# Performance work log

Measured on AMD Instinct MI355X. Metric: run time of the kernel, lower is better.

## Reference

```python
import jax, jax.numpy as jnp
import numpy as np

N = 50000          # nodes
E = 1250000        # edges (no self loops in raw data)
H = 2              # heads
C = 32             # out channels per head
DIN = 64           # dim_node
ED = 16            # edge_dim
G = 16             # graphs in batch
NC = 5             # num classes
SLOPE = 0.2        # GATConv leaky_relu negative_slope


def _glorot(key, shape):
    fan = shape[0] if len(shape) == 2 else shape[-1]
    return jax.random.normal(key, shape, jnp.float32) * (1.0 / np.sqrt(fan))


def setup_inputs() -> dict:
    key = jax.random.key(0)
    ks = jax.random.split(key, 24)
    x = jax.random.normal(ks[0], (N, DIN), jnp.float32)
    dst = jax.random.randint(ks[1], (E,), 0, N)
    off = jax.random.randint(ks[2], (E,), 1, N)
    src = (dst + off) % N  # guarantees src != dst (PyG removes self loops before re-adding)
    edge_index = jnp.stack([src, dst]).astype(jnp.int32)
    edge_attr = jax.random.normal(ks[3], (E, ED), jnp.float32)
    batch = jnp.sort(jax.random.randint(ks[4], (N,), 0, G)).astype(jnp.int32)
    inp = dict(x=x, edge_index=edge_index, edge_attr=edge_attr, batch=batch)
    # layer 1: in=DIN, heads=H, out=C, concat -> H*C
    inp["W1"] = _glorot(ks[5], (DIN, H * C)); inp["asrc1"] = _glorot(ks[6], (H, C))
    inp["adst1"] = _glorot(ks[7], (H, C)); inp["We1"] = _glorot(ks[8], (ED, H * C))
    inp["ae1"] = _glorot(ks[9], (H, C)); inp["b1"] = jnp.zeros((H * C,), jnp.float32)
    # layer 2: in=H*C, heads=H, out=C, concat
    inp["W2"] = _glorot(ks[10], (H * C, H * C)); inp["asrc2"] = _glorot(ks[11], (H, C))
    inp["adst2"] = _glorot(ks[12], (H, C)); inp["We2"] = _glorot(ks[13], (ED, H * C))
    inp["ae2"] = _glorot(ks[14], (H, C)); inp["b2"] = jnp.zeros((H * C,), jnp.float32)
    # layer 3: in=H*C, heads=1, out=C, concat=False
    inp["W3"] = _glorot(ks[15], (H * C, C)); inp["asrc3"] = _glorot(ks[16], (1, C))
    inp["adst3"] = _glorot(ks[17], (1, C)); inp["We3"] = _glorot(ks[18], (ED, C))
    inp["ae3"] = _glorot(ks[19], (1, C)); inp["b3"] = jnp.zeros((C,), jnp.float32)
    # ffn: Linear(C, NC) + softmax (dropout is identity in eval)
    inp["Wf"] = _glorot(ks[20], (C, NC)); inp["bf"] = jnp.zeros((NC,), jnp.float32)
    return inp


def _gat_layer(h_in, src, dst, eattr, W, asrc, adst, We, ae, b, heads, out, concat):
    n = h_in.shape[0]
    h = (h_in @ W).reshape(n, heads, out)                      # [N,H,C]
    s_src = jnp.einsum('nhc,hc->nh', h, asrc)                  # per-node src scores
    s_dst = jnp.einsum('nhc,hc->nh', h, adst)
    he = (eattr @ We).reshape(-1, heads, out)                  # [E,H,C]
    s_e = jnp.einsum('ehc,hc->eh', he, ae)
    logit = jax.nn.leaky_relu(s_src[src] + s_dst[dst] + s_e, SLOPE)  # [E,H]
    m = jax.ops.segment_max(logit, dst, num_segments=n)
    ex = jnp.exp(logit - m[dst])
    den = jax.ops.segment_sum(ex, dst, num_segments=n)
    alpha = ex / (den[dst] + 1e-16)                            # segment softmax per dst node
    agg = jax.ops.segment_sum(h[src] * alpha[..., None], dst, num_segments=n)  # [N,H,C]
    out_x = agg.reshape(n, heads * out) if concat else agg.mean(axis=1)
    return out_x + b


def _gat_forward(x, edge_index, edge_attr, batch,
                 W1, asrc1, adst1, We1, ae1, b1,
                 W2, asrc2, adst2, We2, ae2, b2,
                 W3, asrc3, adst3, We3, ae3, b3,
                 Wf, bf):
    src, dst = edge_index[0], edge_index[1]
    n = x.shape[0]
    # add_self_loops with fill_value='mean': self-loop edge_attr = mean of incoming edge_attr
    deg = jax.ops.segment_sum(jnp.ones((src.shape[0],), x.dtype), dst, num_segments=n)
    self_attr = jax.ops.segment_sum(edge_attr, dst, num_segments=n) / jnp.maximum(deg, 1.0)[:, None]
    loop = jnp.arange(n, dtype=src.dtype)
    src_a = jnp.concatenate([src, loop])
    dst_a = jnp.concatenate([dst, loop])
    eattr_a = jnp.concatenate([edge_attr, self_attr], axis=0)

    h = jax.nn.relu(_gat_layer(x, src_a, dst_a, eattr_a, W1, asrc1, adst1, We1, ae1, b1, H, C, True))
    h = jax.nn.relu(_gat_layer(h, src_a, dst_a, eattr_a, W2, asrc2, adst2, We2, ae2, b2, H, C, True))
    h = jax.nn.relu(_gat_layer(h, src_a, dst_a, eattr_a, W3, asrc3, adst3, We3, ae3, b3, 1, C, False))

    # global mean pool per graph
    cnt = jax.ops.segment_sum(jnp.ones((n,), h.dtype), batch, num_segments=G)
    pooled = jax.ops.segment_sum(h, batch, num_segments=G) / jnp.maximum(cnt, 1.0)[:, None]
    # ffn: Dropout (identity at eval) -> Linear -> Softmax(dim=1)
    return jax.nn.softmax(pooled @ Wf + bf, axis=1)


def reference(x, edge_index, edge_attr, batch,
              W1, asrc1, adst1, We1, ae1, b1,
              W2, asrc2, adst2, We2, ae2, b2,
              W3, asrc3, adst3, We3, ae3, b3,
              Wf, bf):
    return _gat_forward(x, edge_index, edge_attr, batch,
                        W1, asrc1, adst1, We1, ae1, b1,
                        W2, asrc2, adst2, We2, ae2, b2,
                        W3, asrc3, adst3, We3, ae3, b3,
                        Wf, bf)
```

## Files before the change

kernel.cpp:

```cpp
#include <hip/hip_runtime.h>
#include <math.h>

#define NN 50000
#define EE 1250000
#define GG 16
#define NCLS 5
#define NBIN 391
#define BINSHIFT 7
#define CAPB 3900
#define NABLK 153
#define NTBLK 3125

constexpr size_t AL(size_t x){ return (x + 255) & ~size_t(255); }
constexpr size_t OFF_ROWPTR = 0;
constexpr size_t OFF_SRCS   = OFF_ROWPTR + AL((size_t)(NN+1)*4);
constexpr size_t OFF_SE12   = OFF_SRCS + AL((size_t)EE*2);
constexpr size_t OFF_SE34   = OFF_SE12 + AL((size_t)EE*4);
constexpr size_t OFF_SE5    = OFF_SE34 + AL((size_t)EE*4);
constexpr size_t OFF_SSRCA  = OFF_SE5 + AL((size_t)EE*2);
constexpr size_t OFF_SDSTA  = OFF_SSRCA + AL((size_t)NN*2*4);
constexpr size_t OFF_SSRCB  = OFF_SDSTA + AL((size_t)NN*2*4);
constexpr size_t OFF_SDSTB  = OFF_SSRCB + AL((size_t)NN*2*4);
constexpr size_t OFF_STAG   = OFF_SDSTB + AL((size_t)NN*2*4);
constexpr size_t OFF_BUFHA  = OFF_STAG + AL((size_t)NBIN*CAPB*16);
constexpr size_t OFF_BUFHB  = OFF_BUFHA + AL((size_t)NN*32*4);
constexpr size_t OFF_BUFO   = OFF_BUFHB + AL((size_t)NN*32*4);
constexpr size_t OFF_POOL   = OFF_BUFO + AL((size_t)NN*32*4);

__device__ __forceinline__ float leaky(float x){ return x > 0.f ? x : 0.2f*x; }
__device__ __forceinline__ unsigned rne_bf16(float x){
    unsigned u = __float_as_uint(x);
    return (u + 0x7FFFu + ((u >> 16) & 1u)) >> 16;
}
__device__ __forceinline__ float bf16lo(unsigned p){ return __uint_as_float(p << 16); }
__device__ __forceinline__ float bf16hi(unsigned p){ return __uint_as_float(p & 0xFFFF0000u); }

__global__ __launch_bounds__(1024)
void binAt1_kernel(const int* __restrict__ src, const int* __restrict__ dst,
                   const float* __restrict__ eattr,
                   const float* __restrict__ We1, const float* __restrict__ ae1,
                   const float* __restrict__ We2, const float* __restrict__ ae2,
                   const float* __restrict__ We3, const float* __restrict__ ae3,
                   int* __restrict__ bincursor, int4* __restrict__ staging,
                   const float* __restrict__ x, const float* __restrict__ W1,
                   const float* __restrict__ asrc1, const float* __restrict__ adst1,
                   unsigned* __restrict__ hout2, float* __restrict__ ssrc,
                   float* __restrict__ sdst, int nE, int nN){
    __shared__ float smem[5120];
    int tid = threadIdx.x;

    if (blockIdx.x >= NABLK){
        float* Ws  = smem;
        float* ins = smem + 4096;
        for (int i = tid; i < 4096; i += 1024) Ws[i] = W1[i];
        int base = (blockIdx.x - NABLK) * 16;
        {
            int n = base + (tid >> 6);
            ins[tid] = (n < nN) ? x[(size_t)n*64 + (tid & 63)] : 0.f;
        }
        __syncthreads();
        int r = tid >> 6, c = tid & 63;
        int n = base + r;
        float acc = 0.f;
        #pragma unroll
        for (int d = 0; d < 64; ++d) acc += ins[r*64 + d] * Ws[d*64 + c];
        float ps = acc * asrc1[c];
        float pd = acc * adst1[c];
        #pragma unroll
        for (int m = 1; m <= 16; m <<= 1){ ps += __shfl_xor(ps, m); pd += __shfl_xor(pd, m); }
        float accN = __shfl_xor(acc, 1);
        if (n < nN){
            if ((c & 1) == 0){
                unsigned pk = rne_bf16(acc) | (rne_bf16(accN) << 16);
                hout2[(size_t)n*32 + (c >> 1)] = pk;
            }
            if ((c & 31) == 0){
                int h = c >> 5;
                ssrc[n*2 + h] = ps;
                sdst[n*2 + h] = pd;
            }
        }
        return;
    }

    int*   lcount = (int*)smem;
    int*   lbase  = lcount + NBIN;
    float* w      = (float*)(lbase + NBIN);
    if (tid < 80){
        int j = tid >> 4, d = tid & 15;
        const float* We; const float* ae; int hc, h;
        if (j == 0){ We = We1; ae = ae1; hc = 64; h = 0; }
        else if (j == 1){ We = We1; ae = ae1; hc = 64; h = 1; }
        else if (j == 2){ We = We2; ae = ae2; hc = 64; h = 0; }
        else if (j == 3){ We = We2; ae = ae2; hc = 64; h = 1; }
        else { We = We3; ae = ae3; hc = 32; h = 0; }
        float s = 0.f;
        for (int c = 0; c < 32; ++c) s += We[d*hc + h*32 + c] * ae[h*32 + c];
        w[tid] = s;
    }
    for (int i = tid; i < NBIN; i += 1024) lcount[i] = 0;
    __syncthreads();
    int base = blockIdx.x * 8192;
    int w0[8], bn[8], idx[8]; unsigned p01[8], p23[8], p4[8];
    #pragma unroll
    for (int k = 0; k < 8; ++k){
        int i = base + k*1024 + tid;
        if (i < nE){
            int d = dst[i];
            int s = src[i];
            bn[k]  = d >> BINSHIFT;
            w0[k]  = s | ((d & 127) << 16);
            const float4* row = (const float4*)(eattr + (size_t)i*16);
            float4 a0 = row[0], a1 = row[1], a2 = row[2], a3 = row[3];
            float a[16] = {a0.x,a0.y,a0.z,a0.w, a1.x,a1.y,a1.z,a1.w,
                           a2.x,a2.y,a2.z,a2.w, a3.x,a3.y,a3.z,a3.w};
            float sj[5];
            #pragma unroll
            for (int j = 0; j < 5; ++j){
                float s2 = 0.f;
                #pragma unroll
                for (int d2 = 0; d2 < 16; ++d2) s2 += a[d2]*w[j*16+d2];
                sj[j] = s2;
            }
            p01[k] = rne_bf16(sj[0]) | (rne_bf16(sj[1]) << 16);
            p23[k] = rne_bf16(sj[2]) | (rne_bf16(sj[3]) << 16);
            p4[k]  = rne_bf16(sj[4]);
            idx[k] = atomicAdd(&lcount[bn[k]], 1);
        } else bn[k] = -1;
    }
    __syncthreads();
    for (int i = tid; i < NBIN; i += 1024){
        int c = lcount[i];
        lbase[i] = c ? (i*CAPB + atomicAdd(&bincursor[i], c)) : 0;
    }
    __syncthreads();
    #pragma unroll
    for (int k = 0; k < 8; ++k)
        if (bn[k] >= 0)
            staging[lbase[bn[k]] + idx[k]] = make_int4(w0[k], (int)p01[k], (int)p23[k], (int)p4[k]);
}

__global__ void binB_kernel(const int* __restrict__ bincursor, const int4* __restrict__ staging,
                            unsigned short* __restrict__ srcs, unsigned* __restrict__ se12,
                            unsigned* __restrict__ se34, unsigned short* __restrict__ se5,
                            int* __restrict__ rowptr, int nN){
    __shared__ int4 lout[CAPB];
    __shared__ int lcnt[128];
    __shared__ int lpre[128];
    __shared__ int sbb;
    int b = blockIdx.x;
    int sbase = b*CAPB;
    int cnt = bincursor[b];
    int tid = threadIdx.x;
    if (tid < 128) lcnt[tid] = 0;
    if (tid < 64){
        int sum = 0;
        for (int i = tid; i < b; i += 64) sum += bincursor[i];
        #pragma unroll
        for (int m = 1; m < 64; m <<= 1) sum += __shfl_xor(sum, m);
        if (tid == 0) sbb = sum;
    }
    __syncthreads();
    for (int k = tid; k < cnt; k += 1024)
        atomicAdd(&lcnt[staging[sbase + k].x >> 16], 1);
    __syncthreads();
    if (tid < 64){
        int a0 = lcnt[2*tid], a1 = lcnt[2*tid+1];
        int pair = a0 + a1, incl = pair;
        #pragma unroll
        for (int off = 1; off < 64; off <<= 1){
            int t = __shfl_up(incl, off);
            if (tid >= off) incl += t;
        }
        int base0 = incl - pair;
        lpre[2*tid] = base0;
        lpre[2*tid+1] = base0 + a0;
    }
    __syncthreads();
    int r0 = sbb;
    int lo = b << BINSHIFT;
    if (tid < 128 && lo + tid < nN) rowptr[lo + tid] = r0 + lpre[tid];
    if (b == 0 && tid == 0) rowptr[nN] = EE;
    if (tid < 128) lcnt[tid] = 0;
    __syncthreads();
    for (int k = tid; k < cnt; k += 1024){
        int4 v = staging[sbase + k];
        int dl = v.x >> 16;
        int rank = atomicAdd(&lcnt[dl], 1);
        v.x &= 0xFFFF;
        lout[lpre[dl] + rank] = v;
    }
    __syncthreads();
    for (int k = tid; k < cnt; k += 1024){
        int4 v = lout[k];
        srcs[r0 + k] = (unsigned short)v.x;
        se12[r0 + k] = (unsigned)v.y;
        se34[r0 + k] = (unsigned)v.z;
        se5[r0 + k]  = (unsigned short)v.w;
    }
}

template<int NEXTC>
__global__ __launch_bounds__(1024)
void agg64f_kernel(const int* __restrict__ rowptr, const unsigned short* __restrict__ srcs,
                   const unsigned* __restrict__ sePa,
                   const float* __restrict__ ssrc, const float* __restrict__ sdst,
                   const unsigned* __restrict__ hbuf2, const float* __restrict__ bias,
                   const float* __restrict__ Wn, const float* __restrict__ asrcn,
                   const float* __restrict__ adstn,
                   unsigned* __restrict__ houtn, float* __restrict__ ssrcn,
                   float* __restrict__ sdstn, int nN){
    __shared__ float WnS[64*NEXTC];
    __shared__ float os[16*64];
    int tid = threadIdx.x;
    int wid = tid >> 6;
    int lane = tid & 63;
    for (int i = tid; i < 64*NEXTC; i += 1024) WnS[i] = Wn[i];
    int n = blockIdx.x*16 + wid;

    int row_start = rowptr[n], row_end = rowptr[n+1];
    int degn = row_end - row_start;
    float sd0 = sdst[n*2 + 0];
    float sd1 = sdst[n*2 + 1];
    int sub = lane >> 4;
    int lc  = lane & 15;
    int h   = lc >> 3;
    float acc0=0.f, acc1=0.f, acc2=0.f, acc3=0.f, den=0.f;
    float ssp0=0.f, ssp1=0.f;
    const uint2* hb2 = (const uint2*)hbuf2;

    for (int p0 = row_start; p0 < row_end; p0 += 64){
        int myp = p0 + lane;
        int srcreg = 0; unsigned wpk = 0;
        if (myp < row_end){
            srcreg = srcs[myp];
            unsigned pk = sePa[myp];
            float e0 = bf16lo(pk);
            float e1 = bf16hi(pk);
            ssp0 += e0; ssp1 += e1;
            float2 sv = ((const float2*)ssrc)[srcreg];
            float w0 = __expf(leaky(sv.x + sd0 + e0));
            float w1 = __expf(leaky(sv.y + sd1 + e1));
            wpk = rne_bf16(w0) | (rne_bf16(w1) << 16);
        }
        int cnt = min(64, row_end - p0);
        #pragma unroll 4
        for (int q = sub; q < cnt; q += 4){
            int sj = __shfl(srcreg, q);
            unsigned wq = __shfl(wpk, q);
            float wj = h ? bf16hi(wq) : bf16lo(wq);
            den += wj;
            uint2 hv = hb2[(size_t)sj*16 + lc];
            acc0 += wj * bf16lo(hv.x);
            acc1 += wj * bf16hi(hv.x);
            acc2 += wj * bf16lo(hv.y);
            acc3 += wj * bf16hi(hv.y);
        }
    }
    #pragma unroll
    for (int m = 16; m < 64; m <<= 1){
        acc0 += __shfl_xor(acc0, m); acc1 += __shfl_xor(acc1, m);
        acc2 += __shfl_xor(acc2, m); acc3 += __shfl_xor(acc3, m);
        den  += __shfl_xor(den, m);
    }
    #pragma unroll
    for (int m = 1; m < 64; m <<= 1){
        ssp0 += __shfl_xor(ssp0, m);
        ssp1 += __shfl_xor(ssp1, m);
    }
    float invdeg = 1.f / (float)max(degn, 1);
    float srh = ssrc[n*2 + h];
    float sdh = h ? sd1 : sd0;
    float ssh = h ? ssp1 : ssp0;
    float wself = __expf(leaky(srh + sdh + ssh*invdeg));
    uint2 hv = hb2[(size_t)n*16 + lc];
    acc0 += wself * bf16lo(hv.x); acc1 += wself * bf16hi(hv.x);
    acc2 += wself * bf16lo(hv.y); acc3 += wself * bf16hi(hv.y);
    den += wself;
    if (lane < 16){
        float inv = 1.f / (den + 1e-16f);
        os[wid*64 + 4*lc+0] = fmaxf(acc0*inv + bias[4*lc+0], 0.f);
        os[wid*64 + 4*lc+1] = fmaxf(acc1*inv + bias[4*lc+1], 0.f);
        os[wid*64 + 4*lc+2] = fmaxf(acc2*inv + bias[4*lc+2], 0.f);
        os[wid*64 + 4*lc+3] = fmaxf(acc3*inv + bias[4*lc+3], 0.f);
    }
    __syncthreads();
    if (NEXTC == 64){
        int c = lane;
        float hh = 0.f;
        #pragma unroll
        for (int d = 0; d < 64; ++d) hh += os[wid*64 + d] * WnS[d*64 + c];
        float ps = hh * asrcn[c];
        float pd = hh * adstn[c];
        #pragma unroll
        for (int m = 1; m <= 16; m <<= 1){ ps += __shfl_xor(ps, m); pd += __shfl_xor(pd, m); }
        float hN = __shfl_xor(hh, 1);
        if ((c & 1) == 0){
            unsigned pk = rne_bf16(hh) | (rne_bf16(hN) << 16);
            houtn[(size_t)n*32 + (c >> 1)] = pk;
        }
        if ((c & 31) == 0){
            int hh2 = c >> 5;
            ssrcn[n*2 + hh2] = ps;
            sdstn[n*2 + hh2] = pd;
        }
    } else {
        int c = lane & 31, dh = lane >> 5;
        float part = 0.f;
        #pragma unroll
        for (int d = 0; d < 32; ++d) part += os[wid*64 + dh*32 + d] * WnS[(dh*32 + d)*32 + c];
        float hh = part + __shfl_xor(part, 32);
        float ps = hh * asrcn[c];
        float pd = hh * adstn[c];
        #pragma unroll
        for (int m = 1; m <= 16; m <<= 1){ ps += __shfl_xor(ps, m); pd += __shfl_xor(pd, m); }
        float hN = __shfl_xor(hh, 1);
        if (lane < 32 && (c & 1) == 0){
            unsigned pk = rne_bf16(hh) | (rne_bf16(hN) << 16);
            houtn[(size_t)n*16 + (c >> 1)] = pk;
        }
        if (lane == 0){ ssrcn[n] = ps; sdstn[n] = pd; }
    }
}

__global__ void agg32_kernel(const int* __restrict__ rowptr, const unsigned short* __restrict__ srcs,
                             const unsigned short* __restrict__ sePb,
                             const float* __restrict__ ssrc, const float* __restrict__ sdst,
                             const unsigned* __restrict__ hbuf2, const float* __restrict__ bias,
                             float* __restrict__ outbuf, int nN){
    int wid = threadIdx.x >> 6;
    int lane = threadIdx.x & 63;
    int n = blockIdx.x*4 + wid;
    if (n >= nN) return;
    int row_start = rowptr[n], row_end = rowptr[n+1];
    int degn = row_end - row_start;
    float sd0 = sdst[n];
    int sub = lane >> 3;
    int lc  = lane & 7;
    float acc0=0.f, acc1=0.f, acc2=0.f, acc3=0.f, den=0.f, ssp0=0.f;
    const uint2* hb2 = (const uint2*)hbuf2;

    for (int p0 = row_start; p0 < row_end; p0 += 64){
        int myp = p0 + lane;
        int srcreg = 0; float w0s = 0.f;
        if (myp < row_end){
            srcreg = srcs[myp];
            float e0 = __uint_as_float(((unsigned)sePb[myp]) << 16);
            ssp0 += e0;
            w0s = __expf(leaky(ssrc[srcreg] + sd0 + e0));
        }
        int cnt = min(64, row_end - p0);
        #pragma unroll 4
        for (int q = sub; q < cnt; q += 8){
            int sj = __shfl(srcreg, q);
            float wj = __shfl(w0s, q);
            den += wj;
            uint2 hv = hb2[(size_t)sj*8 + lc];
            acc0 += wj * bf16lo(hv.x);
            acc1 += wj * bf16hi(hv.x);
            acc2 += wj * bf16lo(hv.y);
            acc3 += wj * bf16hi(hv.y);
        }
    }
    #pragma unroll
    for (int m = 8; m < 64; m <<= 1){
        acc0 += __shfl_xor(acc0, m); acc1 += __shfl_xor(acc1, m);
        acc2 += __shfl_xor(acc2, m); acc3 += __shfl_xor(acc3, m);
        den  += __shfl_xor(den, m);
    }
    #pragma unroll
    for (int m = 1; m < 64; m <<= 1) ssp0 += __shfl_xor(ssp0, m);
    float invdeg = 1.f / (float)max(degn, 1);
    float wself = __expf(leaky(ssrc[n] + sd0 + ssp0*invdeg));
    uint2 hv = hb2[(size_t)n*8 + lc];
    acc0 += wself * bf16lo(hv.x); acc1 += wself * bf16hi(hv.x);
    acc2 += wself * bf16lo(hv.y); acc3 += wself * bf16hi(hv.y);
    den += wself;
    if (lane < 8){
        float inv = 1.f / (den + 1e-16f);
        float4 o;
        o.x = fmaxf(acc0*inv + bias[4*lc+0], 0.f);
        o.y = fmaxf(acc1*inv + bias[4*lc+1], 0.f);
        o.z = fmaxf(acc2*inv + bias[4*lc+2], 0.f);
        o.w = fmaxf(acc3*inv + bias[4*lc+3], 0.f);
        ((float4*)outbuf)[(size_t)n*8 + lc] = o;
    }
}

__global__ void pool_kernel(const float* __restrict__ h3, const int* __restrict__ batch,
                            float* __restrict__ pool, float* __restrict__ cnt, int nN){
    __shared__ float accs[GG*32];
    __shared__ float acccnt[GG];
    int tid = threadIdx.x;
    for (int i = tid; i < GG*32; i += 256) accs[i] = 0.f;
    if (tid < GG) acccnt[tid] = 0.f;
    __syncthreads();
    int r = tid >> 5, c = tid & 31;
    int base = blockIdx.x * 512;
    int end = min(base + 512, nN);
    for (int n = base + r; n < end; n += 8){
        int g = batch[n];
        atomicAdd(&accs[g*32 + c], h3[(size_t)n*32 + c]);
        if (c == 0) atomicAdd(&acccnt[g], 1.f);
    }
    __syncthreads();
    for (int i = tid; i < GG*32; i += 256) atomicAdd(&pool[i], accs[i]);
    if (tid < GG) atomicAdd(&cnt[tid], acccnt[tid]);
}

__global__ void final_kernel(const float* __restrict__ pool, const float* __restrict__ cnt,
                             const float* __restrict__ Wf, const float* __restrict__ bf,
                             float* __restrict__ out){
    int g = threadIdx.x;
    if (g >= GG) return;
    float ic = 1.f / fmaxf(cnt[g], 1.f);
    float lg[NCLS];
    #pragma unroll
    for (int k = 0; k < NCLS; ++k) lg[k] = bf[k];
    for (int c = 0; c < 32; ++c){
        float v = pool[g*32 + c] * ic;
        #pragma unroll
        for (int k = 0; k < NCLS; ++k) lg[k] += v * Wf[c*NCLS + k];
    }
    float mx = lg[0];
    #pragma unroll
    for (int k = 1; k < NCLS; ++k) mx = fmaxf(mx, lg[k]);
    float sum = 0.f, ex[NCLS];
    #pragma unroll
    for (int k = 0; k < NCLS; ++k){ ex[k] = expf(lg[k] - mx); sum += ex[k]; }
    #pragma unroll
    for (int k = 0; k < NCLS; ++k) out[g*NCLS + k] = ex[k]/sum;
}

extern "C" void kernel_launch(void* const* d_in, const int* in_sizes, int n_in,
                              void* d_out, int out_size, void* d_ws, size_t ws_size,
                              hipStream_t stream){
    const float* x     = (const float*)d_in[0];
    const int*   eidx  = (const int*)d_in[1];
    const float* eattr = (const float*)d_in[2];
    const int*   batch = (const int*)d_in[3];
    const float* W1 = (const float*)d_in[4];  const float* asrc1 = (const float*)d_in[5];
    const float* adst1 = (const float*)d_in[6]; const float* We1 = (const float*)d_in[7];
    const float* ae1 = (const float*)d_in[8];  const float* b1 = (const float*)d_in[9];
    const float* W2 = (const float*)d_in[10]; const float* asrc2 = (const float*)d_in[11];
    const float* adst2 = (const float*)d_in[12]; const float* We2 = (const float*)d_in[13];
    const float* ae2 = (const float*)d_in[14]; const float* b2 = (const float*)d_in[15];
    const float* W3 = (const float*)d_in[16]; const float* asrc3 = (const float*)d_in[17];
    const float* adst3 = (const float*)d_in[18]; const float* We3 = (const float*)d_in[19];
    const float* ae3 = (const float*)d_in[20]; const float* b3 = (const float*)d_in[21];
    const float* Wf = (const float*)d_in[22]; const float* bf = (const float*)d_in[23];
    float* out = (float*)d_out;

    char* ws = (char*)d_ws;
    int*   rowptr = (int*)(ws + OFF_ROWPTR);
    unsigned short* srcs = (unsigned short*)(ws + OFF_SRCS);
    unsigned* se12 = (unsigned*)(ws + OFF_SE12);
    unsigned* se34 = (unsigned*)(ws + OFF_SE34);
    unsigned short* se5 = (unsigned short*)(ws + OFF_SE5);
    float* ssrcA  = (float*)(ws + OFF_SSRCA);
    float* sdstA  = (float*)(ws + OFF_SDSTA);
    float* ssrcB  = (float*)(ws + OFF_SSRCB);
    float* sdstB  = (float*)(ws + OFF_SDSTB);
    int4*  staging = (int4*)(ws + OFF_STAG);
    unsigned* bufHA = (unsigned*)(ws + OFF_BUFHA);
    unsigned* bufHB = (unsigned*)(ws + OFF_BUFHB);
    float* bufO   = (float*)(ws + OFF_BUFO);
    float* pool   = (float*)(ws + OFF_POOL);
    float* cnt    = pool + GG*32;
    int*   bincursor = (int*)(cnt + GG);

    const int* srcA = eidx;
    const int* dstA = eidx + EE;

    hipMemsetAsync(pool, 0, (GG*32 + GG)*4 + NBIN*4, stream);

    binAt1_kernel<<<NABLK + NTBLK, 1024, 0, stream>>>(srcA, dstA, eattr,
                                                      We1, ae1, We2, ae2, We3, ae3,
                                                      bincursor, staging,
                                                      x, W1, asrc1, adst1,
                                                      bufHA, ssrcA, sdstA, EE, NN);
    binB_kernel<<<NBIN, 1024, 0, stream>>>(bincursor, staging, srcs, se12, se34, se5, rowptr, NN);

    agg64f_kernel<64><<<NTBLK, 1024, 0, stream>>>(rowptr, srcs, se12, ssrcA, sdstA,
                                                  bufHA, b1, W2, asrc2, adst2,
                                                  bufHB, ssrcB, sdstB, NN);
    agg64f_kernel<32><<<NTBLK, 1024, 0, stream>>>(rowptr, srcs, se34, ssrcB, sdstB,
                                                  bufHB, b2, W3, asrc3, adst3,
                                                  bufHA, ssrcA, sdstA, NN);
    agg32_kernel<<<(NN + 3)/4, 256, 0, stream>>>(rowptr, srcs, se5, ssrcA, sdstA,
                                                 bufHA, b3, bufO, NN);
    pool_kernel<<<(NN + 511)/512, 256, 0, stream>>>(bufO, batch, pool, cnt, NN);
    final_kernel<<<1, 64, 0, stream>>>(pool, cnt, Wf, bf, out);
}
```

Baseline: 257.4 us.

## Group nodes by in-degree so aggregation waves process similar-degree nodes

Builds an in-degree histogram in the CSR build kernel, then adds a single-block kernel that counting-sorts node ids into degree buckets. The three aggregation kernels read their node id through this order array, so the wavefronts in a block handle nodes of similar degree and load imbalance within a block shrinks. In exchange it adds a serial single-block kernel launch over 50k nodes with shared-memory atomics, one extra indirection per node, and scattered rather than contiguous access to rowptr, sdst and the output rows.

```diff
diff --git a/kernel.cpp b/kernel.cpp
--- a/kernel.cpp
+++ b/kernel.cpp
@@ -25,7 +25,8 @@
 constexpr size_t OFF_BUFHA  = OFF_STAG + AL((size_t)NBIN*CAPB*16);
 constexpr size_t OFF_BUFHB  = OFF_BUFHA + AL((size_t)NN*32*4);
 constexpr size_t OFF_BUFO   = OFF_BUFHB + AL((size_t)NN*32*4);
-constexpr size_t OFF_POOL   = OFF_BUFO + AL((size_t)NN*32*4);
+constexpr size_t OFF_ORDER  = OFF_BUFO + AL((size_t)NN*32*4);
+constexpr size_t OFF_POOL   = OFF_ORDER + AL((size_t)NN*4);
 
 __device__ __forceinline__ float leaky(float x){ return x > 0.f ? x : 0.2f*x; }
 __device__ __forceinline__ unsigned rne_bf16(float x){
@@ -143,7 +144,7 @@
 __global__ void binB_kernel(const int* __restrict__ bincursor, const int4* __restrict__ staging,
                             unsigned short* __restrict__ srcs, unsigned* __restrict__ se12,
                             unsigned* __restrict__ se34, unsigned short* __restrict__ se5,
-                            int* __restrict__ rowptr, int nN){
+                            int* __restrict__ rowptr, int* __restrict__ deghist, int nN){
     __shared__ int4 lout[CAPB];
     __shared__ int lcnt[128];
     __shared__ int lpre[128];
@@ -179,7 +180,10 @@
     __syncthreads();
     int r0 = sbb;
     int lo = b << BINSHIFT;
-    if (tid < 128 && lo + tid < nN) rowptr[lo + tid] = r0 + lpre[tid];
+    if (tid < 128 && lo + tid < nN){
+        rowptr[lo + tid] = r0 + lpre[tid];
+        atomicAdd(&deghist[min(lcnt[tid], 255)], 1);
+    }
     if (b == 0 && tid == 0) rowptr[nN] = EE;
     if (tid < 128) lcnt[tid] = 0;
     __syncthreads();
@@ -200,9 +204,32 @@
     }
 }
 
+__global__ void order_kernel(const int* __restrict__ deghist, const int* __restrict__ rowptr,
+                             int* __restrict__ order, int nN){
+    __shared__ int lcur[256];
+    int tid = threadIdx.x;
+    int hv = (tid < 256) ? deghist[tid] : 0;
+    if (tid < 256) lcur[tid] = hv;
+    __syncthreads();
+    for (int off = 1; off < 256; off <<= 1){
+        int t = (tid >= off && tid < 256) ? lcur[tid - off] : 0;
+        __syncthreads();
+        if (tid < 256) lcur[tid] += t;
+        __syncthreads();
+    }
+    if (tid < 256) lcur[tid] -= hv;
+    __syncthreads();
+    for (int n = tid; n < nN; n += 1024){
+        int deg = rowptr[n+1] - rowptr[n];
+        int pos = atomicAdd(&lcur[min(deg, 255)], 1);
+        order[pos] = n;
+    }
+}
+
 template<int NEXTC>
 __global__ __launch_bounds__(1024)
-void agg64f_kernel(const int* __restrict__ rowptr, const unsigned short* __restrict__ srcs,
+void agg64f_kernel(const int* __restrict__ order,
+                   const int* __restrict__ rowptr, const unsigned short* __restrict__ srcs,
                    const unsigned* __restrict__ sePa,
                    const float* __restrict__ ssrc, const float* __restrict__ sdst,
                    const unsigned* __restrict__ hbuf2, const float* __restrict__ bias,
@@ -216,7 +243,7 @@
     int wid = tid >> 6;
     int lane = tid & 63;
     for (int i = tid; i < 64*NEXTC; i += 1024) WnS[i] = Wn[i];
-    int n = blockIdx.x*16 + wid;
+    int n = order[blockIdx.x*16 + wid];
 
     int row_start = rowptr[n], row_end = rowptr[n+1];
     int degn = row_end - row_start;
@@ -323,15 +350,17 @@
     }
 }
 
-__global__ void agg32_kernel(const int* __restrict__ rowptr, const unsigned short* __restrict__ srcs,
+__global__ void agg32_kernel(const int* __restrict__ order,
+                             const int* __restrict__ rowptr, const unsigned short* __restrict__ srcs,
                              const unsigned short* __restrict__ sePb,
                              const float* __restrict__ ssrc, const float* __restrict__ sdst,
                              const unsigned* __restrict__ hbuf2, const float* __restrict__ bias,
                              float* __restrict__ outbuf, int nN){
     int wid = threadIdx.x >> 6;
     int lane = threadIdx.x & 63;
-    int n = blockIdx.x*4 + wid;
-    if (n >= nN) return;
+    int gid = blockIdx.x*4 + wid;
+    if (gid >= nN) return;
+    int n = order[gid];
     int row_start = rowptr[n], row_end = rowptr[n+1];
     int degn = row_end - row_start;
     float sd0 = sdst[n];
@@ -465,29 +494,33 @@
     unsigned* bufHA = (unsigned*)(ws + OFF_BUFHA);
     unsigned* bufHB = (unsigned*)(ws + OFF_BUFHB);
     float* bufO   = (float*)(ws + OFF_BUFO);
+    int*   order  = (int*)(ws + OFF_ORDER);
     float* pool   = (float*)(ws + OFF_POOL);
     float* cnt    = pool + GG*32;
     int*   bincursor = (int*)(cnt + GG);
+    int*   deghist   = bincursor + NBIN;
 
     const int* srcA = eidx;
     const int* dstA = eidx + EE;
 
-    hipMemsetAsync(pool, 0, (GG*32 + GG)*4 + NBIN*4, stream);
+    hipMemsetAsync(pool, 0, (GG*32 + GG)*4 + (NBIN + 256)*4, stream);
 
     binAt1_kernel<<<NABLK + NTBLK, 1024, 0, stream>>>(srcA, dstA, eattr,
                                                       We1, ae1, We2, ae2, We3, ae3,
                                                       bincursor, staging,
                                                       x, W1, asrc1, adst1,
                                                       bufHA, ssrcA, sdstA, EE, NN);
-    binB_kernel<<<NBIN, 1024, 0, stream>>>(bincursor, staging, srcs, se12, se34, se5, rowptr, NN);
-
-    agg64f_kernel<64><<<NTBLK, 1024, 0, stream>>>(rowptr, srcs, se12, ssrcA, sdstA,
+    binB_kernel<<<NBIN, 1024, 0, stream>>>(bincursor, staging, srcs, se12, se34, se5,
+                                           rowptr, deghist, NN);
+    order_kernel<<<1, 1024, 0, stream>>>(deghist, rowptr, order, NN);
+
+    agg64f_kernel<64><<<NTBLK, 1024, 0, stream>>>(order, rowptr, srcs, se12, ssrcA, sdstA,
                                                   bufHA, b1, W2, asrc2, adst2,
                                                   bufHB, ssrcB, sdstB, NN);
-    agg64f_kernel<32><<<NTBLK, 1024, 0, stream>>>(rowptr, srcs, se34, ssrcB, sdstB,
+    agg64f_kernel<32><<<NTBLK, 1024, 0, stream>>>(order, rowptr, srcs, se34, ssrcB, sdstB,
                                                   bufHB, b2, W3, asrc3, adst3,
                                                   bufHA, ssrcA, sdstA, NN);
-    agg32_kernel<<<(NN + 3)/4, 256, 0, stream>>>(rowptr, srcs, se5, ssrcA, sdstA,
+    agg32_kernel<<<(NN + 3)/4, 256, 0, stream>>>(order, rowptr, srcs, se5, ssrcA, sdstA,
                                                  bufHA, b3, bufO, NN);
     pool_kernel<<<(NN + 511)/512, 256, 0, stream>>>(bufO, batch, pool, cnt, NN);
     final_kernel<<<1, 64, 0, stream>>>(pool, cnt, Wf, bf, out);
```

Result: slower. 406.8 us (+58.1%).

## Fuse final aggregation with mean pooling and split layer-1 transform out of binning

Applied to the files above, without the earlier changes.

Folds global mean pooling into the last GAT aggregation kernel, so per-node outputs go into shared-memory per-graph accumulators and are flushed with global atomics. This removes the intermediate output buffer and the separate pool launch. It also splits the layer-1 node transform out of the fused binning kernel into its own 4-node-per-block kernel, trading one fused launch for two simpler ones. The risk is that the 12,500 blocks each issue up to 528 global atomics, which may contend on the 16 graph rows.

```diff
diff --git a/kernel.cpp b/kernel.cpp
--- a/kernel.cpp
+++ b/kernel.cpp
@@ -24,8 +24,7 @@
 constexpr size_t OFF_STAG   = OFF_SDSTB + AL((size_t)NN*2*4);
 constexpr size_t OFF_BUFHA  = OFF_STAG + AL((size_t)NBIN*CAPB*16);
 constexpr size_t OFF_BUFHB  = OFF_BUFHA + AL((size_t)NN*32*4);
-constexpr size_t OFF_BUFO   = OFF_BUFHB + AL((size_t)NN*32*4);
-constexpr size_t OFF_POOL   = OFF_BUFO + AL((size_t)NN*32*4);
+constexpr size_t OFF_POOL   = OFF_BUFHB + AL((size_t)NN*32*4);
 
 __device__ __forceinline__ float leaky(float x){ return x > 0.f ? x : 0.2f*x; }
 __device__ __forceinline__ unsigned rne_bf16(float x){
@@ -36,56 +35,16 @@
 __device__ __forceinline__ float bf16hi(unsigned p){ return __uint_as_float(p & 0xFFFF0000u); }
 
 __global__ __launch_bounds__(1024)
-void binAt1_kernel(const int* __restrict__ src, const int* __restrict__ dst,
-                   const float* __restrict__ eattr,
-                   const float* __restrict__ We1, const float* __restrict__ ae1,
-                   const float* __restrict__ We2, const float* __restrict__ ae2,
-                   const float* __restrict__ We3, const float* __restrict__ ae3,
-                   int* __restrict__ bincursor, int4* __restrict__ staging,
-                   const float* __restrict__ x, const float* __restrict__ W1,
-                   const float* __restrict__ asrc1, const float* __restrict__ adst1,
-                   unsigned* __restrict__ hout2, float* __restrict__ ssrc,
-                   float* __restrict__ sdst, int nE, int nN){
-    __shared__ float smem[5120];
+void binA_kernel(const int* __restrict__ src, const int* __restrict__ dst,
+                 const float* __restrict__ eattr,
+                 const float* __restrict__ We1, const float* __restrict__ ae1,
+                 const float* __restrict__ We2, const float* __restrict__ ae2,
+                 const float* __restrict__ We3, const float* __restrict__ ae3,
+                 int* __restrict__ bincursor, int4* __restrict__ staging, int nE){
+    __shared__ int lcount[NBIN];
+    __shared__ int lbase[NBIN];
+    __shared__ float w[80];
     int tid = threadIdx.x;
-
-    if (blockIdx.x >= NABLK){
-        float* Ws  = smem;
-        float* ins = smem + 4096;
-        for (int i = tid; i < 4096; i += 1024) Ws[i] = W1[i];
-        int base = (blockIdx.x - NABLK) * 16;
-        {
-            int n = base + (tid >> 6);
-            ins[tid] = (n < nN) ? x[(size_t)n*64 + (tid & 63)] : 0.f;
-        }
-        __syncthreads();
-        int r = tid >> 6, c = tid & 63;
-        int n = base + r;
-        float acc = 0.f;
-        #pragma unroll
-        for (int d = 0; d < 64; ++d) acc += ins[r*64 + d] * Ws[d*64 + c];
-        float ps = acc * asrc1[c];
-        float pd = acc * adst1[c];
-        #pragma unroll
-        for (int m = 1; m <= 16; m <<= 1){ ps += __shfl_xor(ps, m); pd += __shfl_xor(pd, m); }
-        float accN = __shfl_xor(acc, 1);
-        if (n < nN){
-            if ((c & 1) == 0){
-                unsigned pk = rne_bf16(acc) | (rne_bf16(accN) << 16);
-                hout2[(size_t)n*32 + (c >> 1)] = pk;
-            }
-            if ((c & 31) == 0){
-                int h = c >> 5;
-                ssrc[n*2 + h] = ps;
-                sdst[n*2 + h] = pd;
-            }
-        }
-        return;
-    }
-
-    int*   lcount = (int*)smem;
-    int*   lbase  = lcount + NBIN;
-    float* w      = (float*)(lbase + NBIN);
     if (tid < 80){
         int j = tid >> 4, d = tid & 15;
         const float* We; const float* ae; int hc, h;
@@ -140,6 +99,43 @@
             staging[lbase[bn[k]] + idx[k]] = make_int4(w0[k], (int)p01[k], (int)p23[k], (int)p4[k]);
 }
 
+__global__ void transform1_kernel(const float* __restrict__ in, const float* __restrict__ W,
+                                  const float* __restrict__ asrc, const float* __restrict__ adst,
+                                  unsigned* __restrict__ hout2, float* __restrict__ ssrc,
+                                  float* __restrict__ sdst, int nN){
+    __shared__ float Ws[64*64];
+    __shared__ float ins[4*64];
+    int tid = threadIdx.x;
+    for (int i = tid; i < 4096; i += 256) Ws[i] = W[i];
+    int base = blockIdx.x * 4;
+    for (int i = tid; i < 256; i += 256){
+        int n = base + i/64;
+        ins[i] = (n < nN) ? in[(size_t)n*64 + (i & 63)] : 0.f;
+    }
+    __syncthreads();
+    int r = tid >> 6, c = tid & 63;
+    int n = base + r;
+    float acc = 0.f;
+    #pragma unroll
+    for (int d = 0; d < 64; ++d) acc += ins[r*64 + d] * Ws[d*64 + c];
+    float ps = acc * asrc[c];
+    float pd = acc * adst[c];
+    #pragma unroll
+    for (int m = 1; m <= 16; m <<= 1){ ps += __shfl_xor(ps, m); pd += __shfl_xor(pd, m); }
+    float accN = __shfl_xor(acc, 1);
+    if (n < nN){
+        if ((c & 1) == 0){
+            unsigned pk = rne_bf16(acc) | (rne_bf16(accN) << 16);
+            hout2[(size_t)n*32 + (c >> 1)] = pk;
+        }
+        if ((c & 31) == 0){
+            int h = c >> 5;
+            ssrc[n*2 + h] = ps;
+            sdst[n*2 + h] = pd;
+        }
+    }
+}
+
 __global__ void binB_kernel(const int* __restrict__ bincursor, const int4* __restrict__ staging,
                             unsigned short* __restrict__ srcs, unsigned* __restrict__ se12,
                             unsigned* __restrict__ se34, unsigned short* __restrict__ se5,
@@ -323,89 +319,79 @@
     }
 }
 
-__global__ void agg32_kernel(const int* __restrict__ rowptr, const unsigned short* __restrict__ srcs,
-                             const unsigned short* __restrict__ sePb,
-                             const float* __restrict__ ssrc, const float* __restrict__ sdst,
-                             const unsigned* __restrict__ hbuf2, const float* __restrict__ bias,
-                             float* __restrict__ outbuf, int nN){
-    int wid = threadIdx.x >> 6;
-    int lane = threadIdx.x & 63;
-    int n = blockIdx.x*4 + wid;
-    if (n >= nN) return;
-    int row_start = rowptr[n], row_end = rowptr[n+1];
-    int degn = row_end - row_start;
-    float sd0 = sdst[n];
-    int sub = lane >> 3;
-    int lc  = lane & 7;
-    float acc0=0.f, acc1=0.f, acc2=0.f, acc3=0.f, den=0.f, ssp0=0.f;
-    const uint2* hb2 = (const uint2*)hbuf2;
-
-    for (int p0 = row_start; p0 < row_end; p0 += 64){
-        int myp = p0 + lane;
-        int srcreg = 0; float w0s = 0.f;
-        if (myp < row_end){
-            srcreg = srcs[myp];
-            float e0 = __uint_as_float(((unsigned)sePb[myp]) << 16);
-            ssp0 += e0;
-            w0s = __expf(leaky(ssrc[srcreg] + sd0 + e0));
-        }
-        int cnt = min(64, row_end - p0);
-        #pragma unroll 4
-        for (int q = sub; q < cnt; q += 8){
-            int sj = __shfl(srcreg, q);
-            float wj = __shfl(w0s, q);
-            den += wj;
-            uint2 hv = hb2[(size_t)sj*8 + lc];
-            acc0 += wj * bf16lo(hv.x);
-            acc1 += wj * bf16hi(hv.x);
-            acc2 += wj * bf16lo(hv.y);
-            acc3 += wj * bf16hi(hv.y);
-        }
-    }
-    #pragma unroll
-    for (int m = 8; m < 64; m <<= 1){
-        acc0 += __shfl_xor(acc0, m); acc1 += __shfl_xor(acc1, m);
-        acc2 += __shfl_xor(acc2, m); acc3 += __shfl_xor(acc3, m);
-        den  += __shfl_xor(den, m);
-    }
-    #pragma unroll
-    for (int m = 1; m < 64; m <<= 1) ssp0 += __shfl_xor(ssp0, m);
-    float invdeg = 1.f / (float)max(degn, 1);
-    float wself = __expf(leaky(ssrc[n] + sd0 + ssp0*invdeg));
-    uint2 hv = hb2[(size_t)n*8 + lc];
-    acc0 += wself * bf16lo(hv.x); acc1 += wself * bf16hi(hv.x);
-    acc2 += wself * bf16lo(hv.y); acc3 += wself * bf16hi(hv.y);
-    den += wself;
-    if (lane < 8){
-        float inv = 1.f / (den + 1e-16f);
-        float4 o;
-        o.x = fmaxf(acc0*inv + bias[4*lc+0], 0.f);
-        o.y = fmaxf(acc1*inv + bias[4*lc+1], 0.f);
-        o.z = fmaxf(acc2*inv + bias[4*lc+2], 0.f);
-        o.w = fmaxf(acc3*inv + bias[4*lc+3], 0.f);
-        ((float4*)outbuf)[(size_t)n*8 + lc] = o;
-    }
-}
-
-__global__ void pool_kernel(const float* __restrict__ h3, const int* __restrict__ batch,
-                            float* __restrict__ pool, float* __restrict__ cnt, int nN){
+__global__ void agg32p_kernel(const int* __restrict__ rowptr, const unsigned short* __restrict__ srcs,
+                              const unsigned short* __restrict__ sePb,
+                              const float* __restrict__ ssrc, const float* __restrict__ sdst,
+                              const unsigned* __restrict__ hbuf2, const float* __restrict__ bias,
+                              const int* __restrict__ batch,
+                              float* __restrict__ pool, float* __restrict__ cnt, int nN){
     __shared__ float accs[GG*32];
     __shared__ float acccnt[GG];
     int tid = threadIdx.x;
     for (int i = tid; i < GG*32; i += 256) accs[i] = 0.f;
     if (tid < GG) acccnt[tid] = 0.f;
     __syncthreads();
-    int r = tid >> 5, c = tid & 31;
-    int base = blockIdx.x * 512;
-    int end = min(base + 512, nN);
-    for (int n = base + r; n < end; n += 8){
-        int g = batch[n];
-        atomicAdd(&accs[g*32 + c], h3[(size_t)n*32 + c]);
-        if (c == 0) atomicAdd(&acccnt[g], 1.f);
-    }
-    __syncthreads();
-    for (int i = tid; i < GG*32; i += 256) atomicAdd(&pool[i], accs[i]);
-    if (tid < GG) atomicAdd(&cnt[tid], acccnt[tid]);
+    int wid = tid >> 6;
+    int lane = tid & 63;
+    int n = blockIdx.x*4 + wid;
+    if (n < nN){
+        int row_start = rowptr[n], row_end = rowptr[n+1];
+        int degn = row_end - row_start;
+        float sd0 = sdst[n];
+        int sub = lane >> 3;
+        int lc  = lane & 7;
+        float acc0=0.f, acc1=0.f, acc2=0.f, acc3=0.f, den=0.f, ssp0=0.f;
+        const uint2* hb2 = (const uint2*)hbuf2;
+
+        for (int p0 = row_start; p0 < row_end; p0 += 64){
+            int myp = p0 + lane;
+            int srcreg = 0; float w0s = 0.f;
+            if (myp < row_end){
+                srcreg = srcs[myp];
+                float e0 = __uint_as_float(((unsigned)sePb[myp]) << 16);
+                ssp0 += e0;
+                w0s = __expf(leaky(ssrc[srcreg] + sd0 + e0));
+            }
+            int cnt2 = min(64, row_end - p0);
+            #pragma unroll 4
+            for (int q = sub; q < cnt2; q += 8){
+                int sj = __shfl(srcreg, q);
+                float wj = __shfl(w0s, q);
+                den += wj;
+                uint2 hv = hb2[(size_t)sj*8 + lc];
+                acc0 += wj * bf16lo(hv.x);
+                acc1 += wj * bf16hi(hv.x);
+                acc2 += wj * bf16lo(hv.y);
+                acc3 += wj * bf16hi(hv.y);
+            }
+        }
+        #pragma unroll
+        for (int m = 8; m < 64; m <<= 1){
+            acc0 += __shfl_xor(acc0, m); acc1 += __shfl_xor(acc1, m);
+            acc2 += __shfl_xor(acc2, m); acc3 += __shfl_xor(acc3, m);
+            den  += __shfl_xor(den, m);
+        }
+        #pragma unroll
+        for (int m = 1; m < 64; m <<= 1) ssp0 += __shfl_xor(ssp0, m);
+        float invdeg = 1.f / (float)max(degn, 1);
+        float wself = __expf(leaky(ssrc[n] + sd0 + ssp0*invdeg));
+        uint2 hv = hb2[(size_t)n*8 + lc];
+        acc0 += wself * bf16lo(hv.x); acc1 += wself * bf16hi(hv.x);
+        acc2 += wself * bf16lo(hv.y); acc3 += wself * bf16hi(hv.y);
+        den += wself;
+        if (lane < 8){
+            float inv = 1.f / (den + 1e-16f);
+            int g = batch[n];
+            atomicAdd(&accs[g*32 + 4*lc+0], fmaxf(acc0*inv + bias[4*lc+0], 0.f));
+            atomicAdd(&accs[g*32 + 4*lc+1], fmaxf(acc1*inv + bias[4*lc+1], 0.f));
+            atomicAdd(&accs[g*32 + 4*lc+2], fmaxf(acc2*inv + bias[4*lc+2], 0.f));
+            atomicAdd(&accs[g*32 + 4*lc+3], fmaxf(acc3*inv + bias[4*lc+3], 0.f));
+            if (lc == 0) atomicAdd(&acccnt[g], 1.f);
+        }
+    }
+    __syncthreads();
+    for (int i = tid; i < GG*32; i += 256) if (accs[i] != 0.f) atomicAdd(&pool[i], accs[i]);
+    if (tid < GG && acccnt[tid] != 0.f) atomicAdd(&cnt[tid], acccnt[tid]);
 }
 
 __global__ void final_kernel(const float* __restrict__ pool, const float* __restrict__ cnt,
@@ -464,7 +450,6 @@
     int4*  staging = (int4*)(ws + OFF_STAG);
     unsigned* bufHA = (unsigned*)(ws + OFF_BUFHA);
     unsigned* bufHB = (unsigned*)(ws + OFF_BUFHB);
-    float* bufO   = (float*)(ws + OFF_BUFO);
     float* pool   = (float*)(ws + OFF_POOL);
     float* cnt    = pool + GG*32;
     int*   bincursor = (int*)(cnt + GG);
@@ -474,12 +459,13 @@
 
     hipMemsetAsync(pool, 0, (GG*32 + GG)*4 + NBIN*4, stream);
 
-    binAt1_kernel<<<NABLK + NTBLK, 1024, 0, stream>>>(srcA, dstA, eattr,
-                                                      We1, ae1, We2, ae2, We3, ae3,
-                                                      bincursor, staging,
-                                                      x, W1, asrc1, adst1,
-                                                      bufHA, ssrcA, sdstA, EE, NN);
-    binB_kernel<<<NBIN, 1024, 0, stream>>>(bincursor, staging, srcs, se12, se34, se5, rowptr, NN);
+    binA_kernel<<<NABLK, 1024, 0, stream>>>(srcA, dstA, eattr,
+                                            We1, ae1, We2, ae2, We3, ae3,
+                                            bincursor, staging, EE);
+    transform1_kernel<<<(NN + 3)/4, 256, 0, stream>>>(x, W1, asrc1, adst1,
+                                                      bufHA, ssrcA, sdstA, NN);
+    binB_kernel<<<NBIN, 1024, 0, stream>>>(bincursor, staging, srcs, se12, se34, se5,
+                                           rowptr, NN);
 
     agg64f_kernel<64><<<NTBLK, 1024, 0, stream>>>(rowptr, srcs, se12, ssrcA, sdstA,
                                                   bufHA, b1, W2, asrc2, adst2,
@@ -487,8 +473,7 @@
     agg64f_kernel<32><<<NTBLK, 1024, 0, stream>>>(rowptr, srcs, se34, ssrcB, sdstB,
                                                   bufHB, b2, W3, asrc3, adst3,
                                                   bufHA, ssrcA, sdstA, NN);
-    agg32_kernel<<<(NN + 3)/4, 256, 0, stream>>>(rowptr, srcs, se5, ssrcA, sdstA,
-                                                 bufHA, b3, bufO, NN);
-    pool_kernel<<<(NN + 511)/512, 256, 0, stream>>>(bufO, batch, pool, cnt, NN);
+    agg32p_kernel<<<(NN + 3)/4, 256, 0, stream>>>(rowptr, srcs, se5, ssrcA, sdstA,
+                                                  bufHA, b3, batch, pool, cnt, NN);
     final_kernel<<<1, 64, 0, stream>>>(pool, cnt, Wf, bf, out);
 }
```

Result: slower. 375.4 us (+45.9%).
